# Optimization experiments

Measured on AMD Instinct MI355X. Metric: run time of the kernel, lower is better.

The kernel has to match this reference:

```python
import jax, jax.numpy as jnp
import numpy as np

N0, N1, N2, N3, N4, C = 65536, 16384, 4096, 1024, 256, 256


def _linear_params(key, fan_in, fan_out):
    kw, kb = jax.random.split(key)
    lim = 1.0 / np.sqrt(fan_in)
    W = jax.random.uniform(kw, (fan_in, fan_out), minval=-lim, maxval=lim, dtype=jnp.float32)
    b = jax.random.uniform(kb, (fan_out,), minval=-lim, maxval=lim, dtype=jnp.float32)
    return W, b


def setup_inputs() -> dict:
    key = jax.random.key(0)
    ks = jax.random.split(key, 20)
    inp = {
        'xyz0': jax.random.normal(ks[0], (N0, 3), dtype=jnp.float32),
        'idx0': jax.random.randint(ks[1], (N0,), 0, N1),
        'idx1': jax.random.randint(ks[2], (N1,), 0, N0),
        'idx2': jax.random.randint(ks[3], (N2,), 0, N0),
        'idx3': jax.random.randint(ks[4], (N3,), 0, N0),
        'idx4': jax.random.randint(ks[5], (N4,), 0, N0),
    }
    names = ['W_all', 'b_all', 'W4', 'b4', 'W3', 'b3', 'W2', 'b2', 'W1', 'b1', 'W0', 'b0']
    for i in range(6):
        W, b = _linear_params(ks[6 + i], 3, C)
        inp[names[2 * i]] = W
        inp[names[2 * i + 1]] = b
    pnames = ['P4', 'pb4', 'P3', 'pb3', 'P2', 'pb2', 'P1', 'pb1', 'P0', 'pb0']
    for i in range(5):
        W, b = _linear_params(ks[12 + i], 2 * C, C)
        inp[pnames[2 * i]] = W
        inp[pnames[2 * i + 1]] = b
    return inp


def _nn1(xyz, new_xyz):
    # global 1-NN (single batch segment): argmin of squared distance
    d = (jnp.sum(new_xyz ** 2, -1, keepdims=True)
         - 2.0 * new_xyz @ xyz.T
         + jnp.sum(xyz ** 2, -1))  # [M, N]
    return jnp.argmin(d, axis=1)


def _fwd(xyz0, idx0, idx1, idx2, idx3, idx4,
         W_all, b_all, W4, b4, W3, b3, W2, b2, W1, b1, W0, b0,
         P4, pb4, P3, pb3, P2, pb2, P1, pb1, P0, pb0):
    xyz4 = xyz0[idx4]
    xyz3 = xyz0[idx3]
    xyz2 = xyz0[idx2]
    xyz1 = xyz0[idx1]
    f0 = xyz0 @ W_all + b_all          # [N0, C]
    f1, f2, f3, f4 = f0[:N1], f0[:N2], f0[:N3], f0[:N4]
    # level 4: global max pooling as class token (single-batch scatter-amax)
    cls4 = jnp.max(f4, axis=0, keepdims=True)  # [1, C], broadcasts over N4
    f4_nei = cls4 + (xyz4 @ W4 + b4)
    pe4 = jnp.concatenate([f4_nei, f4], axis=-1) @ P4 + pb4
    # level 3
    k34 = _nn1(xyz4, xyz3)
    f3_nei = pe4[k34] + ((xyz3 - xyz4[k34]) @ W3 + b3)
    pe3 = jnp.concatenate([f3_nei, f3], axis=-1) @ P3 + pb3
    # level 2
    k23 = _nn1(xyz3, xyz2)
    f2_nei = pe3[k23] + ((xyz2 - xyz3[k23]) @ W2 + b2)
    pe2 = jnp.concatenate([f2_nei, f2], axis=-1) @ P2 + pb2
    # level 1
    k12 = _nn1(xyz2, xyz1)
    f1_nei = pe2[k12] + ((xyz1 - xyz2[k12]) @ W1 + b1)
    pe1 = jnp.concatenate([f1_nei, f1], axis=-1) @ P1 + pb1
    # level 0: precomputed indices into level 1
    f0_nei = pe1[idx0] + ((xyz0 - xyz1[idx0]) @ W0 + b0)
    pe0 = jnp.concatenate([f0_nei, f0], axis=-1) @ P0 + pb0
    return (pe4, pe3, pe2, pe1, pe0)


def reference(xyz0, idx0, idx1, idx2, idx3, idx4,
              W_all, b_all, W4, b4, W3, b3, W2, b2, W1, b1, W0, b0,
              P4, pb4, P3, pb3, P2, pb2, P1, pb1, P0, pb0):
    return _fwd(xyz0, idx0, idx1, idx2, idx3, idx4,
                W_all, b_all, W4, b4, W3, b3, W2, b2, W1, b1, W0, b0,
                P4, pb4, P3, pb3, P2, pb2, P1, pb1, P0, pb0)
```

## Files before the change

kernel.cpp:

```cpp
#include <hip/hip_runtime.h>
#include <hip/hip_bf16.h>


typedef __hip_bfloat16 bf16;
typedef unsigned short ushort_t;

#define cN0 65536
#define cN1 16384
#define cN2 4096
#define cN3 1024
#define cN4 256

__device__ __forceinline__ float bits2f(ushort_t u) {
    union { unsigned u; float f; } x; x.u = ((unsigned)u) << 16; return x.f;
}
__device__ __forceinline__ float ldf(const void* raw, int fp32, int i) {
    return fp32 ? ((const float*)raw)[i] : bits2f(((const ushort_t*)raw)[i]);
}
__device__ __forceinline__ float3 ld3(const void* raw, int fp32, int i) {
    if (fp32) {
        const float* f = (const float*)raw + 3 * i;
        return make_float3(f[0], f[1], f[2]);
    }
    const ushort_t* u = (const ushort_t*)raw + 3 * i;
    return make_float3(bits2f(u[0]), bits2f(u[1]), bits2f(u[2]));
}

struct RawArgs {
    const void* xyz;
    const void* Wall; const void* ball;
    const void* W[5]; const void* bb[5];
    const void* P[5]; const void* pb[5];
};


__device__ __forceinline__ void nn_body(const void* xyzr, int fp32,
                                        const int* __restrict__ idxQ,
                                        const int* __restrict__ idxR, int nR,
                                        int* __restrict__ outK, int blk,
                                        float4* ref4, float* redD, int* redI) {
    int tid = threadIdx.x;
    int part = tid >> 6;
    int q = blk * 64 + (tid & 63);
    int qi = idxQ[q];
    float3 qv = ld3(xyzr, fp32, qi);
    float qx = qv.x, qy = qv.y, qz = qv.z;
    float q2 = (qx * qx + qy * qy) + qz * qz;
    float best = 3.402823466e38f;
    int bi = 0;
    for (int base = 0; base < nR; base += 1024) {
        int nt = min(1024, nR - base);
        __syncthreads();
        for (int t = tid; t < nt; t += 512) {
            int ri = idxR[base + t];
            float3 r3 = ld3(xyzr, fp32, ri);
            ref4[t] = make_float4(r3.x, r3.y, r3.z,
                                  (r3.x * r3.x + r3.y * r3.y) + r3.z * r3.z);
        }
        __syncthreads();
        int seg = nt >> 3;
        int s0 = part * seg;
        for (int t = 0; t < seg; ++t) {
            float4 rp = ref4[s0 + t];
            float dot = (qx * rp.x + qy * rp.y) + qz * rp.z;
            float d = (q2 - 2.0f * dot) + rp.w;
            if (d < best) { best = d; bi = base + s0 + t; }
        }
    }
    redD[tid] = best;
    redI[tid] = bi;
    __syncthreads();
    if (part == 0) {
#pragma unroll
        for (int p = 1; p < 8; ++p) {
            float d = redD[tid + p * 64];
            int i2 = redI[tid + p * 64];
            if (d < best || (d == best && i2 < bi)) { best = d; bi = i2; }
        }
        outK[q] = bi;
    }
}

__global__ void prep_nn_kernel(RawArgs ra,
                               const int* __restrict__ idx1, const int* __restrict__ idx2,
                               const int* __restrict__ idx3, const int* __restrict__ idx4,
                               float* __restrict__ M1, float* __restrict__ M2,
                               float* __restrict__ cbuf,
                               float* __restrict__ MATS0,
                               int* __restrict__ k34, int* __restrict__ k23,
                               int* __restrict__ k12,
                               int* __restrict__ flag) {
    __shared__ __align__(16) char smem[20608];
    __shared__ int sbad;
    int b = blockIdx.x;
    int tid = threadIdx.x;

    if (tid == 0) sbad = 0;
    __syncthreads();
    {
        const ushort_t* raw0 = (const ushort_t*)ra.xyz;
        for (int i = tid; i < 1024; i += 512) {
            int e = (raw0[i] >> 7) & 0xFF;
            if (e >= 138) atomicOr(&sbad, 1);
        }
    }
    __syncthreads();
    int fp32 = sbad ? 1 : 0;
    if (b == 0 && tid == 0) flag[0] = fp32;

    if (b < 40) {
        int L = b >> 3;
        int tb = b & 7;
        const void* P = ra.P[L];
        const void* W = ra.W[L];
        const void* bvec = ra.bb[L];
        const void* pb = ra.pb[L];
        float* cls4f = (float*)smem;
        float* red = (float*)(smem + 1024);
        float* px = (float*)(smem + 1024 + 7168);
        float* py = px + 256;
        float* pz = py + 256;

        if (L == 0) {
            if (tid < 256) {
                float3 x = ld3(ra.xyz, fp32, tid);
                px[tid] = x.x; py[tid] = x.y; pz[tid] = x.z;
            }
            __syncthreads();
            if (tid < 256) {
                float w0 = ldf(ra.Wall, fp32, tid);
                float w1 = ldf(ra.Wall, fp32, 256 + tid);
                float w2 = ldf(ra.Wall, fp32, 512 + tid);
                float bbv = ldf(ra.ball, fp32, tid);
                float best = -3.402823466e38f;
                for (int i = 0; i < 256; ++i) {
                    float v = fmaf(pz[i], w2, fmaf(py[i], w1, px[i] * w0)) + bbv;
                    best = fmaxf(best, v);
                }
                cls4f[tid] = best;
            }
            __syncthreads();
        }

        if (tid < 256) {
            int j = tid & 31;
            int slice = tid >> 5;
            int col = tb * 32 + j;
            float m10 = 0.f, m11 = 0.f, m12 = 0.f, m20 = 0.f, m21 = 0.f, m22 = 0.f, cc = 0.f;
#pragma unroll 4
            for (int i = 0; i < 32; ++i) {
                int c = slice * 32 + i;
                float pt = ldf(P, fp32, c * 256 + col);
                float pbot = ldf(P, fp32, (256 + c) * 256 + col);
                m10 = fmaf(ldf(W, fp32, c), pt, m10);
                m11 = fmaf(ldf(W, fp32, 256 + c), pt, m11);
                m12 = fmaf(ldf(W, fp32, 512 + c), pt, m12);
                m20 = fmaf(ldf(ra.Wall, fp32, c), pbot, m20);
                m21 = fmaf(ldf(ra.Wall, fp32, 256 + c), pbot, m21);
                m22 = fmaf(ldf(ra.Wall, fp32, 512 + c), pbot, m22);
                cc = fmaf(ldf(bvec, fp32, c), pt, cc);
                cc = fmaf(ldf(ra.ball, fp32, c), pbot, cc);
                if (L == 0) cc = fmaf(cls4f[c], pt, cc);
            }
            red[0 * 256 + tid] = m10; red[1 * 256 + tid] = m11; red[2 * 256 + tid] = m12;
            red[3 * 256 + tid] = m20; red[4 * 256 + tid] = m21; red[5 * 256 + tid] = m22;
            red[6 * 256 + tid] = cc;
        }
        __syncthreads();
        if (tid < 32) {
            int col = tb * 32 + tid;
            float v[7];
#pragma unroll
            for (int q = 0; q < 7; ++q) {
                float s = red[q * 256 + tid];
#pragma unroll
                for (int sl = 1; sl < 8; ++sl) s += red[q * 256 + sl * 32 + tid];
                v[q] = s;
            }
            M1[(size_t)L * 768 + col] = v[0];
            M1[(size_t)L * 768 + 256 + col] = v[1];
            M1[(size_t)L * 768 + 512 + col] = v[2];
            M2[(size_t)L * 768 + col] = v[3];
            M2[(size_t)L * 768 + 256 + col] = v[4];
            M2[(size_t)L * 768 + 512 + col] = v[5];
            float e = v[6] + ldf(pb, fp32, col);
            cbuf[(size_t)L * 256 + col] = e;
            if (L == 0) {
                MATS0[0 * 256 + col] = v[0];
                MATS0[1 * 256 + col] = v[1];
                MATS0[2 * 256 + col] = v[2];
                MATS0[3 * 256 + col] = v[3];
                MATS0[4 * 256 + col] = v[4];
                MATS0[5 * 256 + col] = v[5];
                MATS0[6 * 256 + col] = e;
            }
        }
        return;
    }

    int blk = b - 40;
    float4* ref4 = (float4*)smem;
    float* redD = (float*)(smem + 16384);
    int* redI = (int*)(smem + 18432);
    if (blk < 16)       nn_body(ra.xyz, fp32, idx3, idx4, cN4, k34, blk, ref4, redD, redI);
    else if (blk < 80)  nn_body(ra.xyz, fp32, idx2, idx3, cN3, k23, blk - 16, ref4, redD, redI);
    else                nn_body(ra.xyz, fp32, idx1, idx2, cN2, k12, blk - 80, ref4, redD, redI);
}

__global__ void chain_kernel(const float* __restrict__ inB, int nin_m, int subG0,
                             const void* __restrict__ Praw,
                             const float* __restrict__ G, const float* __restrict__ H,
                             const float* __restrict__ dvec,
                             float* __restrict__ outB, int addMode,
                             const int* __restrict__ flag) {
    __shared__ float srow[256];
    int b = blockIdx.x, col = threadIdx.x;
    int nout = gridDim.x;
    int fp32 = flag[0];

    if (b < nin_m || b == nout - 1) {
        int r = (b == nout - 1) ? nin_m : b;
        srow[col] = inB[r * 256 + col];
        __syncthreads();
        float acc = 0.f;
        for (int c = 0; c < 256; c += 4) {
            float p0 = ldf(Praw, fp32, (c + 0) * 256 + col);
            float p1 = ldf(Praw, fp32, (c + 1) * 256 + col);
            float p2 = ldf(Praw, fp32, (c + 2) * 256 + col);
            float p3 = ldf(Praw, fp32, (c + 3) * 256 + col);
            acc = fmaf(srow[c + 0], p0, acc);
            acc = fmaf(srow[c + 1], p1, acc);
            acc = fmaf(srow[c + 2], p2, acc);
            acc = fmaf(srow[c + 3], p3, acc);
        }
        if (b == nout - 1) acc += dvec[col];
        else if (b >= subG0 && b < subG0 + 3) acc -= G[(b - subG0) * 256 + col];
        outB[b * 256 + col] = acc;
    } else {
        int rr = b - nin_m;
        float v;
        if (addMode) v = G[rr * 256 + col] + H[rr * 256 + col];
        else         v = (rr < 3) ? G[rr * 256 + col] : H[(rr - 3) * 256 + col];
        outB[b * 256 + col] = v;
    }
}

template<int NT>
__device__ __forceinline__ void out_body(
    int row0, size_t off, const float* __restrict__ MB,
    const void* __restrict__ xyz, int fp32,
    const int* __restrict__ idx0, const int* __restrict__ idx1,
    const int* __restrict__ idx2, const int* __restrict__ idx3,
    const int* __restrict__ idx4,
    const int* __restrict__ k34, const int* __restrict__ k23,
    const int* __restrict__ k12,
    void* __restrict__ outv, float (*trips)[28]) {
    int tid = threadIdx.x;
    if (tid < 32) {
        int row = row0 + tid;
        int t[NT];
        if constexpr (NT == 9) {
            int j = idx0[row], k = k12[j], l = k23[k], m = k34[l];
            t[0] = idx4[m]; t[1] = m; t[2] = idx3[l]; t[3] = l;
            t[4] = idx2[k]; t[5] = k; t[6] = idx1[j]; t[7] = j; t[8] = row;
        } else if constexpr (NT == 8) {
            int k = k12[row], l = k23[k], m = k34[l];
            t[0] = idx4[m]; t[1] = m; t[2] = idx3[l]; t[3] = l;
            t[4] = idx2[k]; t[5] = k; t[6] = idx1[row]; t[7] = row;
        } else if constexpr (NT == 6) {
            int l = k23[row], m = k34[l];
            t[0] = idx4[m]; t[1] = m; t[2] = idx3[l]; t[3] = l;
            t[4] = idx2[row]; t[5] = row;
        } else if constexpr (NT == 4) {
            int m = k34[row];
            t[0] = idx4[m]; t[1] = m; t[2] = idx3[row]; t[3] = row;
        } else {
            t[0] = idx4[row]; t[1] = row;
        }
#pragma unroll
        for (int q = 0; q < NT; ++q) {
            float3 x = ld3(xyz, fp32, t[q]);
            trips[tid][3 * q + 0] = x.x;
            trips[tid][3 * q + 1] = x.y;
            trips[tid][3 * q + 2] = x.z;
        }
    }
    int col = tid;
    float M[3 * NT];
#pragma unroll
    for (int r = 0; r < 3 * NT; ++r) M[r] = MB[r * 256 + col];
    float ev = MB[3 * NT * 256 + col];
    __syncthreads();
#pragma unroll 4
    for (int rr = 0; rr < 32; ++rr) {
        float v = ev;
#pragma unroll
        for (int q = 0; q < NT; ++q) {
            v = fmaf(trips[rr][3 * q + 0], M[3 * q + 0], v);
            v = fmaf(trips[rr][3 * q + 1], M[3 * q + 1], v);
            v = fmaf(trips[rr][3 * q + 2], M[3 * q + 2], v);
        }
        size_t idx = off + (size_t)(row0 + rr) * 256 + col;
        if (fp32) ((float*)outv)[idx] = v;
        else      ((bf16*)outv)[idx] = __float2bfloat16(v);
    }
}

__global__ __launch_bounds__(256) void out_kernel(
    const void* __restrict__ xyz,
    const int* __restrict__ idx0, const int* __restrict__ idx1,
    const int* __restrict__ idx2, const int* __restrict__ idx3,
    const int* __restrict__ idx4,
    const int* __restrict__ k34, const int* __restrict__ k23,
    const int* __restrict__ k12,
    const float* __restrict__ MATS,
    const int* __restrict__ flag, void* __restrict__ outv) {
    __shared__ float trips[32][28];
    int b = blockIdx.x;
    int fp32 = flag[0];
    const size_t o4 = 0, o3 = 65536, o2 = 327680, o1 = 1376256, o0 = 5570560;
    if (b < 2048)
        out_body<9>(b * 32, o0, MATS + 4 * 7168, xyz, fp32,
                    idx0, idx1, idx2, idx3, idx4, k34, k23, k12, outv, trips);
    else if (b < 2560)
        out_body<8>((b - 2048) * 32, o1, MATS + 3 * 7168, xyz, fp32,
                    idx0, idx1, idx2, idx3, idx4, k34, k23, k12, outv, trips);
    else if (b < 2688)
        out_body<6>((b - 2560) * 32, o2, MATS + 2 * 7168, xyz, fp32,
                    idx0, idx1, idx2, idx3, idx4, k34, k23, k12, outv, trips);
    else if (b < 2720)
        out_body<4>((b - 2688) * 32, o3, MATS + 1 * 7168, xyz, fp32,
                    idx0, idx1, idx2, idx3, idx4, k34, k23, k12, outv, trips);
    else
        out_body<2>((b - 2720) * 32, o4, MATS + 0 * 7168, xyz, fp32,
                    idx0, idx1, idx2, idx3, idx4, k34, k23, k12, outv, trips);
}

extern "C" void kernel_launch(void* const* d_in, const int* in_sizes, int n_in,
                              void* d_out, int out_size, void* d_ws, size_t ws_size,
                              hipStream_t stream) {
    const int* idx0 = (const int*)d_in[1];
    const int* idx1 = (const int*)d_in[2];
    const int* idx2 = (const int*)d_in[3];
    const int* idx3 = (const int*)d_in[4];
    const int* idx4 = (const int*)d_in[5];

    float* ws = (float*)d_ws;
    int* flag = (int*)ws;
    float* p = ws + 64;
    float* M1buf = p; p += 5 * 768;
    float* M2buf = p; p += 5 * 768;
    float* cbuf = p;  p += 5 * 256;
    int* k34 = (int*)p; p += 1024;
    int* k23 = (int*)p; p += 4096;
    int* k12 = (int*)p; p += 16384;
    float* MATS = p;  p += 5 * 7168;

    RawArgs ra;
    ra.xyz = d_in[0];
    ra.Wall = d_in[6];
    ra.ball = d_in[7];
    for (int i = 0; i < 5; ++i) {
        ra.W[i] = d_in[8 + 2 * i];
        ra.bb[i] = d_in[9 + 2 * i];
        ra.P[i] = d_in[18 + 2 * i];
        ra.pb[i] = d_in[19 + 2 * i];
    }

    prep_nn_kernel<<<376, 512, 0, stream>>>(ra, idx1, idx2, idx3, idx4,
                                            M1buf, M2buf, cbuf, MATS,
                                            k34, k23, k12, flag);

    chain_kernel<<<13, 256, 0, stream>>>(MATS + 0 * 7168, 6, 0, ra.P[1],
                                         M1buf + 1 * 768, M2buf + 1 * 768,
                                         cbuf + 1 * 256, MATS + 1 * 7168, 0, flag);
    chain_kernel<<<19, 256, 0, stream>>>(MATS + 1 * 7168, 12, 6, ra.P[2],
                                         M1buf + 2 * 768, M2buf + 2 * 768,
                                         cbuf + 2 * 256, MATS + 2 * 7168, 0, flag);
    chain_kernel<<<25, 256, 0, stream>>>(MATS + 2 * 7168, 18, 12, ra.P[3],
                                         M1buf + 3 * 768, M2buf + 3 * 768,
                                         cbuf + 3 * 256, MATS + 3 * 7168, 0, flag);
    chain_kernel<<<28, 256, 0, stream>>>(MATS + 3 * 7168, 24, 18, ra.P[4],
                                         M1buf + 4 * 768, M2buf + 4 * 768,
                                         cbuf + 4 * 256, MATS + 4 * 7168, 1, flag);

    out_kernel<<<2728, 256, 0, stream>>>(d_in[0], idx0, idx1, idx2, idx3, idx4,
                                         k34, k23, k12, MATS, flag, d_out);
}
```

Before: 289.2 us.

## Register-tile output kernel 8x8 per thread and split chain K-reduction

The output kernel now processes 64 rows per block. Each thread computes an 8-row by 8-column register tile and writes vectorized float4 or packed 8-wide bf16 stores, replacing per-column scalar stores. Coordinate gathers are spread across all threads through a shared index table. The small chain kernels use 512 threads that split the 256-long dot product in half and reduce through shared memory, shortening the serial loop at the cost of an extra barrier.

Measured after the change: 258.6 us. 1.12x faster.

```diff
diff --git a/kernel.cpp b/kernel.cpp
--- a/kernel.cpp
+++ b/kernel.cpp
@@ -4,6 +4,7 @@
 
 typedef __hip_bfloat16 bf16;
 typedef unsigned short ushort_t;
+typedef __attribute__((ext_vector_type(8))) unsigned short ush8;
 
 #define cN0 65536
 #define cN1 16384
@@ -24,6 +25,12 @@
     }
     const ushort_t* u = (const ushort_t*)raw + 3 * i;
     return make_float3(bits2f(u[0]), bits2f(u[1]), bits2f(u[2]));
+}
+
+__device__ __forceinline__ ushort_t f2b(float v) {
+    union { float f; unsigned u; } x; x.f = v;
+    unsigned r = x.u + 0x7FFF + ((x.u >> 16) & 1);
+    return (ushort_t)(r >> 16);
 }
 
 struct RawArgs {
@@ -32,7 +39,6 @@
     const void* W[5]; const void* bb[5];
     const void* P[5]; const void* pb[5];
 };
-
 
 __device__ __forceinline__ void nn_body(const void* xyzr, int fp32,
                                         const int* __restrict__ idxQ,
@@ -214,16 +220,21 @@
                              float* __restrict__ outB, int addMode,
                              const int* __restrict__ flag) {
     __shared__ float srow[256];
-    int b = blockIdx.x, col = threadIdx.x;
+    __shared__ float sred[2][256];
+    int b = blockIdx.x;
+    int tid = threadIdx.x;
+    int col = tid & 255;
+    int half = tid >> 8;
     int nout = gridDim.x;
     int fp32 = flag[0];
 
     if (b < nin_m || b == nout - 1) {
         int r = (b == nout - 1) ? nin_m : b;
-        srow[col] = inB[r * 256 + col];
+        if (tid < 256) srow[tid] = inB[r * 256 + tid];
         __syncthreads();
         float acc = 0.f;
-        for (int c = 0; c < 256; c += 4) {
+        int c0 = half * 128;
+        for (int c = c0; c < c0 + 128; c += 4) {
             float p0 = ldf(Praw, fp32, (c + 0) * 256 + col);
             float p1 = ldf(Praw, fp32, (c + 1) * 256 + col);
             float p2 = ldf(Praw, fp32, (c + 2) * 256 + col);
@@ -233,10 +244,15 @@
             acc = fmaf(srow[c + 2], p2, acc);
             acc = fmaf(srow[c + 3], p3, acc);
         }
-        if (b == nout - 1) acc += dvec[col];
-        else if (b >= subG0 && b < subG0 + 3) acc -= G[(b - subG0) * 256 + col];
-        outB[b * 256 + col] = acc;
-    } else {
+        sred[half][col] = acc;
+        __syncthreads();
+        if (half == 0) {
+            float a = sred[0][col] + sred[1][col];
+            if (b == nout - 1) a += dvec[col];
+            else if (b >= subG0 && b < subG0 + 3) a -= G[(b - subG0) * 256 + col];
+            outB[b * 256 + col] = a;
+        }
+    } else if (tid < 256) {
         int rr = b - nin_m;
         float v;
         if (addMode) v = G[rr * 256 + col] + H[rr * 256 + col];
@@ -246,7 +262,7 @@
 }
 
 template<int NT>
-__device__ __forceinline__ void out_body(
+__device__ __forceinline__ void out_tile(
     int row0, size_t off, const float* __restrict__ MB,
     const void* __restrict__ xyz, int fp32,
     const int* __restrict__ idx0, const int* __restrict__ idx1,
@@ -254,9 +270,9 @@
     const int* __restrict__ idx4,
     const int* __restrict__ k34, const int* __restrict__ k23,
     const int* __restrict__ k12,
-    void* __restrict__ outv, float (*trips)[28]) {
+    void* __restrict__ outv, int* sidx, float* T) {
     int tid = threadIdx.x;
-    if (tid < 32) {
+    if (tid < 64) {
         int row = row0 + tid;
         int t[NT];
         if constexpr (NT == 9) {
@@ -278,31 +294,62 @@
             t[0] = idx4[row]; t[1] = row;
         }
 #pragma unroll
-        for (int q = 0; q < NT; ++q) {
-            float3 x = ld3(xyz, fp32, t[q]);
-            trips[tid][3 * q + 0] = x.x;
-            trips[tid][3 * q + 1] = x.y;
-            trips[tid][3 * q + 2] = x.z;
-        }
-    }
-    int col = tid;
-    float M[3 * NT];
-#pragma unroll
-    for (int r = 0; r < 3 * NT; ++r) M[r] = MB[r * 256 + col];
-    float ev = MB[3 * NT * 256 + col];
+        for (int q = 0; q < NT; ++q) sidx[tid * 9 + q] = t[q];
+    }
     __syncthreads();
-#pragma unroll 4
-    for (int rr = 0; rr < 32; ++rr) {
-        float v = ev;
-#pragma unroll
-        for (int q = 0; q < NT; ++q) {
-            v = fmaf(trips[rr][3 * q + 0], M[3 * q + 0], v);
-            v = fmaf(trips[rr][3 * q + 1], M[3 * q + 1], v);
-            v = fmaf(trips[rr][3 * q + 2], M[3 * q + 2], v);
-        }
-        size_t idx = off + (size_t)(row0 + rr) * 256 + col;
-        if (fp32) ((float*)outv)[idx] = v;
-        else      ((bf16*)outv)[idx] = __float2bfloat16(v);
+    for (int lin = tid; lin < 64 * NT; lin += 256) {
+        int r = lin / NT, q = lin - r * NT;
+        float3 x = ld3(xyz, fp32, sidx[r * 9 + q]);
+        T[r * 29 + 3 * q + 0] = x.x;
+        T[r * 29 + 3 * q + 1] = x.y;
+        T[r * 29 + 3 * q + 2] = x.z;
+    }
+    __syncthreads();
+    int tc = tid & 31, tr = tid >> 5;
+    int c8 = tc * 8;
+    float4 e0 = *(const float4*)(MB + 3 * NT * 256 + c8);
+    float4 e1 = *(const float4*)(MB + 3 * NT * 256 + c8 + 4);
+    float acc[8][8];
+#pragma unroll
+    for (int i = 0; i < 8; ++i) {
+        acc[i][0] = e0.x; acc[i][1] = e0.y; acc[i][2] = e0.z; acc[i][3] = e0.w;
+        acc[i][4] = e1.x; acc[i][5] = e1.y; acc[i][6] = e1.z; acc[i][7] = e1.w;
+    }
+#pragma unroll 3
+    for (int q2 = 0; q2 < 3 * NT; ++q2) {
+        float4 m0 = *(const float4*)(MB + q2 * 256 + c8);
+        float4 m1 = *(const float4*)(MB + q2 * 256 + c8 + 4);
+        float mv0 = m0.x, mv1 = m0.y, mv2 = m0.z, mv3 = m0.w;
+        float mv4 = m1.x, mv5 = m1.y, mv6 = m1.z, mv7 = m1.w;
+        float tv[8];
+#pragma unroll
+        for (int i = 0; i < 8; ++i) tv[i] = T[(tr * 8 + i) * 29 + q2];
+#pragma unroll
+        for (int i = 0; i < 8; ++i) {
+            acc[i][0] = fmaf(tv[i], mv0, acc[i][0]);
+            acc[i][1] = fmaf(tv[i], mv1, acc[i][1]);
+            acc[i][2] = fmaf(tv[i], mv2, acc[i][2]);
+            acc[i][3] = fmaf(tv[i], mv3, acc[i][3]);
+            acc[i][4] = fmaf(tv[i], mv4, acc[i][4]);
+            acc[i][5] = fmaf(tv[i], mv5, acc[i][5]);
+            acc[i][6] = fmaf(tv[i], mv6, acc[i][6]);
+            acc[i][7] = fmaf(tv[i], mv7, acc[i][7]);
+        }
+    }
+#pragma unroll
+    for (int i = 0; i < 8; ++i) {
+        size_t base = off + (size_t)(row0 + tr * 8 + i) * 256 + c8;
+        if (fp32) {
+            *(float4*)((float*)outv + base) =
+                make_float4(acc[i][0], acc[i][1], acc[i][2], acc[i][3]);
+            *(float4*)((float*)outv + base + 4) =
+                make_float4(acc[i][4], acc[i][5], acc[i][6], acc[i][7]);
+        } else {
+            ush8 pk;
+#pragma unroll
+            for (int j = 0; j < 8; ++j) pk[j] = f2b(acc[i][j]);
+            *(ush8*)((ushort_t*)outv + base) = pk;
+        }
     }
 }
 
@@ -315,25 +362,26 @@
     const int* __restrict__ k12,
     const float* __restrict__ MATS,
     const int* __restrict__ flag, void* __restrict__ outv) {
-    __shared__ float trips[32][28];
+    __shared__ int sidx[64 * 9];
+    __shared__ float T[64 * 29];
     int b = blockIdx.x;
     int fp32 = flag[0];
     const size_t o4 = 0, o3 = 65536, o2 = 327680, o1 = 1376256, o0 = 5570560;
-    if (b < 2048)
-        out_body<9>(b * 32, o0, MATS + 4 * 7168, xyz, fp32,
-                    idx0, idx1, idx2, idx3, idx4, k34, k23, k12, outv, trips);
-    else if (b < 2560)
-        out_body<8>((b - 2048) * 32, o1, MATS + 3 * 7168, xyz, fp32,
-                    idx0, idx1, idx2, idx3, idx4, k34, k23, k12, outv, trips);
-    else if (b < 2688)
-        out_body<6>((b - 2560) * 32, o2, MATS + 2 * 7168, xyz, fp32,
-                    idx0, idx1, idx2, idx3, idx4, k34, k23, k12, outv, trips);
-    else if (b < 2720)
-        out_body<4>((b - 2688) * 32, o3, MATS + 1 * 7168, xyz, fp32,
-                    idx0, idx1, idx2, idx3, idx4, k34, k23, k12, outv, trips);
+    if (b < 1024)
+        out_tile<9>(b * 64, o0, MATS + 4 * 7168, xyz, fp32,
+                    idx0, idx1, idx2, idx3, idx4, k34, k23, k12, outv, sidx, T);
+    else if (b < 1280)
+        out_tile<8>((b - 1024) * 64, o1, MATS + 3 * 7168, xyz, fp32,
+                    idx0, idx1, idx2, idx3, idx4, k34, k23, k12, outv, sidx, T);
+    else if (b < 1344)
+        out_tile<6>((b - 1280) * 64, o2, MATS + 2 * 7168, xyz, fp32,
+                    idx0, idx1, idx2, idx3, idx4, k34, k23, k12, outv, sidx, T);
+    else if (b < 1360)
+        out_tile<4>((b - 1344) * 64, o3, MATS + 1 * 7168, xyz, fp32,
+                    idx0, idx1, idx2, idx3, idx4, k34, k23, k12, outv, sidx, T);
     else
-        out_body<2>((b - 2720) * 32, o4, MATS + 0 * 7168, xyz, fp32,
-                    idx0, idx1, idx2, idx3, idx4, k34, k23, k12, outv, trips);
+        out_tile<2>((b - 1360) * 64, o4, MATS + 0 * 7168, xyz, fp32,
+                    idx0, idx1, idx2, idx3, idx4, k34, k23, k12, outv, sidx, T);
 }
 
 extern "C" void kernel_launch(void* const* d_in, const int* in_sizes, int n_in,
@@ -371,19 +419,19 @@
                                             M1buf, M2buf, cbuf, MATS,
                                             k34, k23, k12, flag);
 
-    chain_kernel<<<13, 256, 0, stream>>>(MATS + 0 * 7168, 6, 0, ra.P[1],
+    chain_kernel<<<13, 512, 0, stream>>>(MATS + 0 * 7168, 6, 0, ra.P[1],
                                          M1buf + 1 * 768, M2buf + 1 * 768,
                                          cbuf + 1 * 256, MATS + 1 * 7168, 0, flag);
-    chain_kernel<<<19, 256, 0, stream>>>(MATS + 1 * 7168, 12, 6, ra.P[2],
+    chain_kernel<<<19, 512, 0, stream>>>(MATS + 1 * 7168, 12, 6, ra.P[2],
                                          M1buf + 2 * 768, M2buf + 2 * 768,
                                          cbuf + 2 * 256, MATS + 2 * 7168, 0, flag);
-    chain_kernel<<<25, 256, 0, stream>>>(MATS + 2 * 7168, 18, 12, ra.P[3],
+    chain_kernel<<<25, 512, 0, stream>>>(MATS + 2 * 7168, 18, 12, ra.P[3],
                                          M1buf + 3 * 768, M2buf + 3 * 768,
                                          cbuf + 3 * 256, MATS + 3 * 7168, 0, flag);
-    chain_kernel<<<28, 256, 0, stream>>>(MATS + 3 * 7168, 24, 18, ra.P[4],
+    chain_kernel<<<28, 512, 0, stream>>>(MATS + 3 * 7168, 24, 18, ra.P[4],
                                          M1buf + 4 * 768, M2buf + 4 * 768,
                                          cbuf + 4 * 256, MATS + 4 * 7168, 1, flag);
 
-    out_kernel<<<2728, 256, 0, stream>>>(d_in[0], idx0, idx1, idx2, idx3, idx4,
+    out_kernel<<<1364, 256, 0, stream>>>(d_in[0], idx0, idx1, idx2, idx3, idx4,
                                          k34, k23, k12, MATS, flag, d_out);
 }
```
